# Optimization experiments

Measured on AMD Instinct MI355X. Metric: run time of the kernel, lower is better.

The kernel has to match this reference:

```python
import jax, jax.numpy as jnp
import numpy as np

B, T, D, H, C = 64, 256, 512, 1024, 1000

def setup_inputs() -> dict:
    key = jax.random.key(0)
    ks = jax.random.split(key, 6)
    s = 1.0 / np.sqrt(H)  # torch nn.RNN init scale
    return {
        "x": jax.random.normal(ks[0], (B, T, D), dtype=jnp.float32),
        "w_ih0": jax.random.normal(ks[1], (H, D), dtype=jnp.float32) * s,
        "w_hh0": jax.random.normal(ks[2], (H, H), dtype=jnp.float32) * s,
        "w_ih1": jax.random.normal(ks[3], (H, H), dtype=jnp.float32) * s,
        "w_hh1": jax.random.normal(ks[4], (H, H), dtype=jnp.float32) * s,
        "w_fc": jax.random.normal(ks[5], (C, H), dtype=jnp.float32) * s,
    }

def _rnn_layer(inp, w_ih, w_hh):
    # inp: [B, T, Din]; ReLU RNN, no bias (matches nn.RNN(nonlinearity='relu', bias=False))
    xs = jnp.einsum('btd,hd->tbh', inp, w_ih)  # precompute input projections for all steps
    h0 = jnp.zeros((inp.shape[0], w_hh.shape[0]), dtype=inp.dtype)
    def step(h, x_t):
        h = jax.nn.relu(x_t + h @ w_hh.T)
        return h, h
    _, ys = jax.lax.scan(step, h0, xs)  # ys: [T, B, H]
    return jnp.swapaxes(ys, 0, 1)  # [B, T, H]

def reference(x, w_ih0, w_hh0, w_ih1, w_hh1, w_fc):
    h1 = _rnn_layer(x, w_ih0, w_hh0)
    h2 = _rnn_layer(h1, w_ih1, w_hh1)
    # fc on last timestep, no bias
    return h2[:, -1, :] @ w_fc.T  # [B, C]
```

## Files before the change

kernel.cpp:

```cpp
#include <hip/hip_runtime.h>

#define T_STEPS 256
#define BATCH   64
#define HID     1024
#define DIN     512
#define NCLS    1000
#define NBLK    128
#define HSZ     (BATCH * HID)
#define POLL_MAX 100000L

typedef __attribute__((ext_vector_type(8))) short  short8;
typedef __attribute__((ext_vector_type(4))) float  f32x4;
typedef unsigned long long u64;

__device__ __forceinline__ unsigned short rne_bf16(float f) {
    unsigned int u = __builtin_bit_cast(unsigned int, f);
    u += 0x7FFFu + ((u >> 16) & 1u);
    return (unsigned short)(u >> 16);
}
__device__ __forceinline__ float bf16_to_f(unsigned short h) {
    unsigned int u = ((unsigned int)h) << 16;
    return __builtin_bit_cast(float, u);
}

#define MFMA(a, b, c) __builtin_amdgcn_mfma_f32_16x16x32_bf16((a), (b), (c), 0, 0, 0)

__device__ __forceinline__ short8 ld_st8(const unsigned short* p) {
    u64 a = __hip_atomic_load((const u64*)p,       __ATOMIC_RELAXED, __HIP_MEMORY_SCOPE_AGENT);
    u64 b = __hip_atomic_load((const u64*)(p + 4), __ATOMIC_RELAXED, __HIP_MEMORY_SCOPE_AGENT);
    union { u64 q[2]; short8 v; } u;
    u.q[0] = a; u.q[1] = b;
    return u.v;
}
__device__ __forceinline__ void st_u32(unsigned short* p, unsigned int v) {
    __hip_atomic_store((unsigned int*)p, v, __ATOMIC_RELAXED, __HIP_MEMORY_SCOPE_AGENT);
}

__device__ __forceinline__ void wave_poll(const int* fa, int ta,
                                          const int* fb, int tb, int lane) {
    const int* f = (lane < 32) ? fa : fb;
    const int  t = (lane < 32) ? ta : tb;
    const int  i = lane & 31;
    for (long it = 0; it < POLL_MAX; ++it) {
        int v = __hip_atomic_load(f + i, __ATOMIC_RELAXED, __HIP_MEMORY_SCOPE_AGENT);
        if (__all(v >= t)) break;
        __builtin_amdgcn_s_sleep(1);
    }
    asm volatile("" ::: "memory");
}

__global__ __launch_bounds__(512, 2)
void rnn_mfma(const float* __restrict__ xproj,
              const unsigned short* __restrict__ whh0h, const unsigned short* __restrict__ whh0l,
              const unsigned short* __restrict__ wih1h, const unsigned short* __restrict__ wih1l,
              const unsigned short* __restrict__ whh1h, const unsigned short* __restrict__ whh1l,
              unsigned short* h1hi, unsigned short* h1lo,
              unsigned short* h2hi, unsigned short* h2lo,
              float* h2f, int* bar) {
    __shared__ float red[8 * 1088];

    const int bid  = blockIdx.x;
    const int tid  = threadIdx.x;
    const int w    = tid >> 6;
    const int lane = tid & 63;
    const int l15  = lane & 15;
    const int kq   = (lane >> 4) * 8;
    const int rm   = tid >> 4;
    const int rn   = (tid * 2) & 31;

    const int isL2 = bid >= 64;
    const int rb   = isL2 ? bid - 64 : bid;
    const int ns   = rb >> 1;
    const int mh   = rb & 1;
    const int nb   = ns * 32;
    const int mb   = mh * 32;

    int* L1f = bar + mh * 32;
    int* L2f = bar + 64 + mh * 32;

    if (!isL2) {
        const int kb = w * 128;
        short8 WH[2][4], WL[2][4];
#pragma unroll
        for (int c = 0; c < 4; ++c)
#pragma unroll
            for (int nt = 0; nt < 2; ++nt) {
                const size_t o = (size_t)(nb + nt * 16 + l15) * HID + kb + c * 32 + kq;
                WH[nt][c] = *(const short8*)(whh0h + o);
                WL[nt][c] = *(const short8*)(whh0l + o);
            }
        for (int p = 0; p < T_STEPS; ++p) {
            const float2 xi = *(const float2*)(xproj + (size_t)p * BATCH * HID +
                                               (size_t)(mb + rm) * HID + nb + rn);
            wave_poll(L1f, p, L2f, p - 3, lane);
            const unsigned short* hch = h1hi + (size_t)(p & 3) * HSZ;
            const unsigned short* hcl = h1lo + (size_t)(p & 3) * HSZ;
            f32x4 acc[2][2] = {};
#pragma unroll
            for (int c = 0; c < 4; ++c) {
                short8 ah[2], al[2];
#pragma unroll
                for (int mt = 0; mt < 2; ++mt) {
                    const size_t o = (size_t)(mb + mt * 16 + l15) * HID + kb + c * 32 + kq;
                    ah[mt] = ld_st8(hch + o);
                    al[mt] = ld_st8(hcl + o);
                }
#pragma unroll
                for (int mt = 0; mt < 2; ++mt)
#pragma unroll
                    for (int nt = 0; nt < 2; ++nt) {
                        acc[mt][nt] = MFMA(ah[mt], WH[nt][c], acc[mt][nt]);
                        acc[mt][nt] = MFMA(al[mt], WH[nt][c], acc[mt][nt]);
                        acc[mt][nt] = MFMA(ah[mt], WL[nt][c], acc[mt][nt]);
                    }
            }
#pragma unroll
            for (int mt = 0; mt < 2; ++mt)
#pragma unroll
                for (int nt = 0; nt < 2; ++nt)
#pragma unroll
                    for (int i = 0; i < 4; ++i)
                        red[w * 1088 + (mt * 16 + (lane >> 4) * 4 + i) * 34 +
                            nt * 16 + l15] = acc[mt][nt][i];
            __syncthreads();
            {
                float s0 = xi.x, s1 = xi.y;
#pragma unroll
                for (int ww = 0; ww < 8; ++ww) {
                    const float* rp = red + ww * 1088 + rm * 34 + rn;
                    s0 += rp[0];
                    s1 += rp[1];
                }
                const float v0 = fmaxf(s0, 0.f), v1 = fmaxf(s1, 0.f);
                const unsigned short h0 = rne_bf16(v0), h1 = rne_bf16(v1);
                const unsigned int hp = (unsigned int)h0 | ((unsigned int)h1 << 16);
                const unsigned int lp = (unsigned int)rne_bf16(v0 - bf16_to_f(h0)) |
                                        ((unsigned int)rne_bf16(v1 - bf16_to_f(h1)) << 16);
                const size_t o  = (size_t)(mb + rm) * HID + nb + rn;
                const size_t ob = (size_t)((p + 1) & 3) * HSZ;
                st_u32(h1hi + ob + o, hp);
                st_u32(h1lo + ob + o, lp);
            }
            __syncthreads();
            if (tid == 0)
                __hip_atomic_store(&L1f[ns], p + 1, __ATOMIC_RELAXED,
                                   __HIP_MEMORY_SCOPE_AGENT);
        }
    } else {
        const unsigned short* ph = (w < 4) ? wih1h : whh1h;
        const unsigned short* pl = (w < 4) ? wih1l : whh1l;
        const int kb = (w & 3) * 256;
        short8 WH[2][8], WL[2][8];
#pragma unroll
        for (int c = 0; c < 8; ++c)
#pragma unroll
            for (int nt = 0; nt < 2; ++nt) {
                const size_t o = (size_t)(nb + nt * 16 + l15) * HID + kb + c * 32 + kq;
                WH[nt][c] = *(const short8*)(ph + o);
                WL[nt][c] = *(const short8*)(pl + o);
            }
        for (int p = 1; p <= T_STEPS; ++p) {
            if (w < 4) wave_poll(L1f, p, L1f, p, lane);
            else       wave_poll(L2f, p - 1, L2f, p - 1, lane);
            const unsigned short* ash = (w < 4) ? h1hi + (size_t)(p & 3) * HSZ
                                                : h2hi + (size_t)((p - 1) & 1) * HSZ;
            const unsigned short* asl = (w < 4) ? h1lo + (size_t)(p & 3) * HSZ
                                                : h2lo + (size_t)((p - 1) & 1) * HSZ;
            f32x4 acc[2][2] = {};
#pragma unroll
            for (int c = 0; c < 8; ++c) {
                short8 ah[2], al[2];
#pragma unroll
                for (int mt = 0; mt < 2; ++mt) {
                    const size_t o = (size_t)(mb + mt * 16 + l15) * HID + kb + c * 32 + kq;
                    ah[mt] = ld_st8(ash + o);
                    al[mt] = ld_st8(asl + o);
                }
#pragma unroll
                for (int mt = 0; mt < 2; ++mt)
#pragma unroll
                    for (int nt = 0; nt < 2; ++nt) {
                        acc[mt][nt] = MFMA(ah[mt], WH[nt][c], acc[mt][nt]);
                        acc[mt][nt] = MFMA(al[mt], WH[nt][c], acc[mt][nt]);
                        acc[mt][nt] = MFMA(ah[mt], WL[nt][c], acc[mt][nt]);
                    }
            }
#pragma unroll
            for (int mt = 0; mt < 2; ++mt)
#pragma unroll
                for (int nt = 0; nt < 2; ++nt)
#pragma unroll
                    for (int i = 0; i < 4; ++i)
                        red[w * 1088 + (mt * 16 + (lane >> 4) * 4 + i) * 34 +
                            nt * 16 + l15] = acc[mt][nt][i];
            __syncthreads();
            {
                float s0 = 0.f, s1 = 0.f;
#pragma unroll
                for (int ww = 0; ww < 8; ++ww) {
                    const float* rp = red + ww * 1088 + rm * 34 + rn;
                    s0 += rp[0];
                    s1 += rp[1];
                }
                const float v0 = fmaxf(s0, 0.f), v1 = fmaxf(s1, 0.f);
                const unsigned short h0 = rne_bf16(v0), h1 = rne_bf16(v1);
                const unsigned int hp = (unsigned int)h0 | ((unsigned int)h1 << 16);
                const unsigned int lp = (unsigned int)rne_bf16(v0 - bf16_to_f(h0)) |
                                        ((unsigned int)rne_bf16(v1 - bf16_to_f(h1)) << 16);
                const size_t o  = (size_t)(mb + rm) * HID + nb + rn;
                const size_t ob = (size_t)(p & 1) * HSZ;
                st_u32(h2hi + ob + o, hp);
                st_u32(h2lo + ob + o, lp);
                if (p == T_STEPS) {
                    float2 f2; f2.x = v0; f2.y = v1;
                    *(float2*)(h2f + o) = f2;
                }
            }
            __syncthreads();
            if (tid == 0)
                __hip_atomic_store(&L2f[ns], p, __ATOMIC_RELAXED,
                                   __HIP_MEMORY_SCOPE_AGENT);
        }
    }
}

__global__ __launch_bounds__(512)
void xproj_gemm(const float* __restrict__ x,
                const unsigned short* __restrict__ wh,
                const unsigned short* __restrict__ wl,
                float* __restrict__ xproj) {
    const int t    = blockIdx.x;
    const int nq   = blockIdx.y;
    const int w    = threadIdx.x >> 6;
    const int lane = threadIdx.x & 63;
    const int l15  = lane & 15;
    const int kq   = (lane >> 4) * 8;
    const int n0   = nq * 256 + w * 32;

    f32x4 acc[4][2] = {};
    for (int c = 0; c < 16; ++c) {
        const int k = c * 32 + kq;
        short8 wfh[2], wfl[2];
#pragma unroll
        for (int nt = 0; nt < 2; ++nt) {
            const size_t o = (size_t)(n0 + nt * 16 + l15) * DIN + k;
            wfh[nt] = *(const short8*)(wh + o);
            wfl[nt] = *(const short8*)(wl + o);
        }
#pragma unroll
        for (int mt = 0; mt < 4; ++mt) {
            const float* xr = x + ((size_t)(mt * 16 + l15) * T_STEPS + t) * DIN + k;
            float4 a0 = *(const float4*)xr;
            float4 a1 = *(const float4*)(xr + 4);
            float f[8] = {a0.x, a0.y, a0.z, a0.w, a1.x, a1.y, a1.z, a1.w};
            short8 ah, al;
#pragma unroll
            for (int i = 0; i < 8; ++i) {
                unsigned short h = rne_bf16(f[i]);
                ah[i] = (short)h;
                al[i] = (short)rne_bf16(f[i] - bf16_to_f(h));
            }
#pragma unroll
            for (int nt = 0; nt < 2; ++nt) {
                acc[mt][nt] = MFMA(ah, wfh[nt], acc[mt][nt]);
                acc[mt][nt] = MFMA(al, wfh[nt], acc[mt][nt]);
                acc[mt][nt] = MFMA(ah, wfl[nt], acc[mt][nt]);
            }
        }
    }
    float* op = xproj + (size_t)t * BATCH * HID;
#pragma unroll
    for (int mt = 0; mt < 4; ++mt)
#pragma unroll
        for (int nt = 0; nt < 2; ++nt)
#pragma unroll
            for (int i = 0; i < 4; ++i) {
                const int m = mt * 16 + (lane >> 4) * 4 + i;
                const int n = n0 + nt * 16 + l15;
                op[(size_t)m * HID + n] = acc[mt][nt][i];
            }
}

__global__ void split_w(const float* __restrict__ src,
                        unsigned short* __restrict__ hi,
                        unsigned short* __restrict__ lo, int n) {
    int i = blockIdx.x * 256 + threadIdx.x;
    if (i < n) {
        float v = src[i];
        unsigned short h = rne_bf16(v);
        hi[i] = h;
        lo[i] = rne_bf16(v - bf16_to_f(h));
    }
}

__global__ void zero_kernel(int* __restrict__ p, int n) {
    int i = blockIdx.x * 256 + threadIdx.x;
    if (i < n) p[i] = 0;
}

__global__ void fc_kernel(const float* __restrict__ h2,
                          const float* __restrict__ w_fc,
                          float* __restrict__ out) {
    __shared__ float hs[HID];
    const int b = blockIdx.x;
    for (int i = threadIdx.x; i < HID; i += 256) hs[i] = h2[(size_t)b * HID + i];
    __syncthreads();
    const int c = blockIdx.y * 256 + threadIdx.x;
    if (c < NCLS) {
        const float* w = w_fc + (size_t)c * HID;
        float s = 0.f;
        for (int k = 0; k < HID; k += 4) {
            float4 wv = *(const float4*)(w + k);
            s += wv.x * hs[k] + wv.y * hs[k + 1] + wv.z * hs[k + 2] + wv.w * hs[k + 3];
        }
        out[(size_t)b * NCLS + c] = s;
    }
}

extern "C" void kernel_launch(void* const* d_in, const int* in_sizes, int n_in,
                              void* d_out, int out_size, void* d_ws, size_t ws_size,
                              hipStream_t stream) {
    const float* x     = (const float*)d_in[0];
    const float* w_ih0 = (const float*)d_in[1];
    const float* w_hh0 = (const float*)d_in[2];
    const float* w_ih1 = (const float*)d_in[3];
    const float* w_hh1 = (const float*)d_in[4];
    const float* w_fc  = (const float*)d_in[5];
    float* out = (float*)d_out;

    char* ws = (char*)d_ws;
    size_t off = 0;
    auto alloc = [&](size_t bytes) { char* p = ws + off; off += bytes; return p; };
    float*          xproj = (float*)alloc((size_t)T_STEPS * BATCH * HID * 4);
    unsigned short* wih0h = (unsigned short*)alloc((size_t)DIN * HID * 2);
    unsigned short* wih0l = (unsigned short*)alloc((size_t)DIN * HID * 2);
    unsigned short* whh0h = (unsigned short*)alloc((size_t)HID * HID * 2);
    unsigned short* whh0l = (unsigned short*)alloc((size_t)HID * HID * 2);
    unsigned short* wih1h = (unsigned short*)alloc((size_t)HID * HID * 2);
    unsigned short* wih1l = (unsigned short*)alloc((size_t)HID * HID * 2);
    unsigned short* whh1h = (unsigned short*)alloc((size_t)HID * HID * 2);
    unsigned short* whh1l = (unsigned short*)alloc((size_t)HID * HID * 2);
    unsigned short* h1hi  = (unsigned short*)alloc(4 * HSZ * 2);
    unsigned short* h1lo  = (unsigned short*)alloc(4 * HSZ * 2);
    unsigned short* h2hi  = (unsigned short*)alloc(2 * HSZ * 2);
    unsigned short* h2lo  = (unsigned short*)alloc(2 * HSZ * 2);
    float*          h2f   = (float*)alloc(HSZ * 4);
    int*            bar   = (int*)alloc(4096);

    split_w<<<(DIN * HID + 255) / 256, 256, 0, stream>>>(w_ih0, wih0h, wih0l, DIN * HID);
    split_w<<<(HID * HID + 255) / 256, 256, 0, stream>>>(w_hh0, whh0h, whh0l, HID * HID);
    split_w<<<(HID * HID + 255) / 256, 256, 0, stream>>>(w_ih1, wih1h, wih1l, HID * HID);
    split_w<<<(HID * HID + 255) / 256, 256, 0, stream>>>(w_hh1, whh1h, whh1l, HID * HID);

    xproj_gemm<<<dim3(T_STEPS, 4), 512, 0, stream>>>(x, wih0h, wih0l, xproj);

    const int nzero = (4 * HSZ * 2 * 2 + 2 * HSZ * 2 * 2 + HSZ * 4 + 4096) / 4;
    zero_kernel<<<(nzero + 255) / 256, 256, 0, stream>>>((int*)h1hi, nzero);

    rnn_mfma<<<NBLK, 512, 0, stream>>>(xproj,
                                       whh0h, whh0l,
                                       wih1h, wih1l, whh1h, whh1l,
                                       h1hi, h1lo, h2hi, h2lo, h2f, bar);

    fc_kernel<<<dim3(64, 4), 256, 0, stream>>>(h2f, w_fc, out);
}
```

Before: 4.424 ms.

## Replace persistent flag-polling RNN kernel with per-step kernel launches

Replaces the single persistent kernel, which synchronized blocks through global flag polling and atomic loads and stores, with 257 launches of a step kernel. Each launch computes layer-1 step k and layer-2 step k-1, so the two layers stay wavefront-pipelined, with stream ordering acting as the barrier. This removes the spin-wait polling and the atomic memory traffic, and shrinks the h1 ring buffer from four slots to two. The cost is per-launch overhead, and each launch must reload the recurrent weights from global memory into registers.

```diff
diff --git a/kernel.cpp b/kernel.cpp
--- a/kernel.cpp
+++ b/kernel.cpp
@@ -7,11 +7,9 @@
 #define NCLS    1000
 #define NBLK    128
 #define HSZ     (BATCH * HID)
-#define POLL_MAX 100000L
 
 typedef __attribute__((ext_vector_type(8))) short  short8;
 typedef __attribute__((ext_vector_type(4))) float  f32x4;
-typedef unsigned long long u64;
 
 __device__ __forceinline__ unsigned short rne_bf16(float f) {
     unsigned int u = __builtin_bit_cast(unsigned int, f);
@@ -25,41 +23,22 @@
 
 #define MFMA(a, b, c) __builtin_amdgcn_mfma_f32_16x16x32_bf16((a), (b), (c), 0, 0, 0)
 
-__device__ __forceinline__ short8 ld_st8(const unsigned short* p) {
-    u64 a = __hip_atomic_load((const u64*)p,       __ATOMIC_RELAXED, __HIP_MEMORY_SCOPE_AGENT);
-    u64 b = __hip_atomic_load((const u64*)(p + 4), __ATOMIC_RELAXED, __HIP_MEMORY_SCOPE_AGENT);
-    union { u64 q[2]; short8 v; } u;
-    u.q[0] = a; u.q[1] = b;
-    return u.v;
-}
-__device__ __forceinline__ void st_u32(unsigned short* p, unsigned int v) {
-    __hip_atomic_store((unsigned int*)p, v, __ATOMIC_RELAXED, __HIP_MEMORY_SCOPE_AGENT);
-}
-
-__device__ __forceinline__ void wave_poll(const int* fa, int ta,
-                                          const int* fb, int tb, int lane) {
-    const int* f = (lane < 32) ? fa : fb;
-    const int  t = (lane < 32) ? ta : tb;
-    const int  i = lane & 31;
-    for (long it = 0; it < POLL_MAX; ++it) {
-        int v = __hip_atomic_load(f + i, __ATOMIC_RELAXED, __HIP_MEMORY_SCOPE_AGENT);
-        if (__all(v >= t)) break;
-        __builtin_amdgcn_s_sleep(1);
-    }
-    asm volatile("" ::: "memory");
-}
-
 __global__ __launch_bounds__(512, 2)
-void rnn_mfma(const float* __restrict__ xproj,
+void rnn_step(int k,
+              const float* __restrict__ xproj,
               const unsigned short* __restrict__ whh0h, const unsigned short* __restrict__ whh0l,
               const unsigned short* __restrict__ wih1h, const unsigned short* __restrict__ wih1l,
               const unsigned short* __restrict__ whh1h, const unsigned short* __restrict__ whh1l,
               unsigned short* h1hi, unsigned short* h1lo,
               unsigned short* h2hi, unsigned short* h2lo,
-              float* h2f, int* bar) {
+              float* h2f) {
     __shared__ float red[8 * 1088];
 
     const int bid  = blockIdx.x;
+    const int isL2 = bid >= 64;
+    if (!isL2 && k >= T_STEPS) return;
+    if (isL2 && k == 0)        return;
+
     const int tid  = threadIdx.x;
     const int w    = tid >> 6;
     const int lane = tid & 63;
@@ -68,15 +47,11 @@
     const int rm   = tid >> 4;
     const int rn   = (tid * 2) & 31;
 
-    const int isL2 = bid >= 64;
-    const int rb   = isL2 ? bid - 64 : bid;
-    const int ns   = rb >> 1;
-    const int mh   = rb & 1;
-    const int nb   = ns * 32;
-    const int mb   = mh * 32;
-
-    int* L1f = bar + mh * 32;
-    int* L2f = bar + 64 + mh * 32;
+    const int rb = isL2 ? bid - 64 : bid;
+    const int ns = rb >> 1;
+    const int mh = rb & 1;
+    const int nb = ns * 32;
+    const int mb = mh * 32;
 
     if (!isL2) {
         const int kb = w * 128;
@@ -89,62 +64,55 @@
                 WH[nt][c] = *(const short8*)(whh0h + o);
                 WL[nt][c] = *(const short8*)(whh0l + o);
             }
-        for (int p = 0; p < T_STEPS; ++p) {
-            const float2 xi = *(const float2*)(xproj + (size_t)p * BATCH * HID +
-                                               (size_t)(mb + rm) * HID + nb + rn);
-            wave_poll(L1f, p, L2f, p - 3, lane);
-            const unsigned short* hch = h1hi + (size_t)(p & 3) * HSZ;
-            const unsigned short* hcl = h1lo + (size_t)(p & 3) * HSZ;
-            f32x4 acc[2][2] = {};
-#pragma unroll
-            for (int c = 0; c < 4; ++c) {
-                short8 ah[2], al[2];
-#pragma unroll
-                for (int mt = 0; mt < 2; ++mt) {
-                    const size_t o = (size_t)(mb + mt * 16 + l15) * HID + kb + c * 32 + kq;
-                    ah[mt] = ld_st8(hch + o);
-                    al[mt] = ld_st8(hcl + o);
+        const float2 xi = *(const float2*)(xproj + (size_t)k * BATCH * HID +
+                                           (size_t)(mb + rm) * HID + nb + rn);
+        const unsigned short* hch = h1hi + (size_t)((k + 1) & 1) * HSZ;
+        const unsigned short* hcl = h1lo + (size_t)((k + 1) & 1) * HSZ;
+        f32x4 acc[2][2] = {};
+#pragma unroll
+        for (int c = 0; c < 4; ++c) {
+            short8 ah[2], al[2];
+#pragma unroll
+            for (int mt = 0; mt < 2; ++mt) {
+                const size_t o = (size_t)(mb + mt * 16 + l15) * HID + kb + c * 32 + kq;
+                ah[mt] = *(const short8*)(hch + o);
+                al[mt] = *(const short8*)(hcl + o);
+            }
+#pragma unroll
+            for (int mt = 0; mt < 2; ++mt)
+#pragma unroll
+                for (int nt = 0; nt < 2; ++nt) {
+                    acc[mt][nt] = MFMA(ah[mt], WH[nt][c], acc[mt][nt]);
+                    acc[mt][nt] = MFMA(al[mt], WH[nt][c], acc[mt][nt]);
+                    acc[mt][nt] = MFMA(ah[mt], WL[nt][c], acc[mt][nt]);
                 }
-#pragma unroll
-                for (int mt = 0; mt < 2; ++mt)
-#pragma unroll
-                    for (int nt = 0; nt < 2; ++nt) {
-                        acc[mt][nt] = MFMA(ah[mt], WH[nt][c], acc[mt][nt]);
-                        acc[mt][nt] = MFMA(al[mt], WH[nt][c], acc[mt][nt]);
-                        acc[mt][nt] = MFMA(ah[mt], WL[nt][c], acc[mt][nt]);
-                    }
-            }
-#pragma unroll
-            for (int mt = 0; mt < 2; ++mt)
-#pragma unroll
-                for (int nt = 0; nt < 2; ++nt)
-#pragma unroll
-                    for (int i = 0; i < 4; ++i)
-                        red[w * 1088 + (mt * 16 + (lane >> 4) * 4 + i) * 34 +
-                            nt * 16 + l15] = acc[mt][nt][i];
-            __syncthreads();
-            {
-                float s0 = xi.x, s1 = xi.y;
-#pragma unroll
-                for (int ww = 0; ww < 8; ++ww) {
-                    const float* rp = red + ww * 1088 + rm * 34 + rn;
-                    s0 += rp[0];
-                    s1 += rp[1];
-                }
-                const float v0 = fmaxf(s0, 0.f), v1 = fmaxf(s1, 0.f);
-                const unsigned short h0 = rne_bf16(v0), h1 = rne_bf16(v1);
-                const unsigned int hp = (unsigned int)h0 | ((unsigned int)h1 << 16);
-                const unsigned int lp = (unsigned int)rne_bf16(v0 - bf16_to_f(h0)) |
-                                        ((unsigned int)rne_bf16(v1 - bf16_to_f(h1)) << 16);
-                const size_t o  = (size_t)(mb + rm) * HID + nb + rn;
-                const size_t ob = (size_t)((p + 1) & 3) * HSZ;
-                st_u32(h1hi + ob + o, hp);
-                st_u32(h1lo + ob + o, lp);
-            }
-            __syncthreads();
-            if (tid == 0)
-                __hip_atomic_store(&L1f[ns], p + 1, __ATOMIC_RELAXED,
-                                   __HIP_MEMORY_SCOPE_AGENT);
+        }
+#pragma unroll
+        for (int mt = 0; mt < 2; ++mt)
+#pragma unroll
+            for (int nt = 0; nt < 2; ++nt)
+#pragma unroll
+                for (int i = 0; i < 4; ++i)
+                    red[w * 1088 + (mt * 16 + (lane >> 4) * 4 + i) * 34 +
+                        nt * 16 + l15] = acc[mt][nt][i];
+        __syncthreads();
+        {
+            float s0 = xi.x, s1 = xi.y;
+#pragma unroll
+            for (int ww = 0; ww < 8; ++ww) {
+                const float* rp = red + ww * 1088 + rm * 34 + rn;
+                s0 += rp[0];
+                s1 += rp[1];
+            }
+            const float v0 = fmaxf(s0, 0.f), v1 = fmaxf(s1, 0.f);
+            const unsigned short h0 = rne_bf16(v0), h1 = rne_bf16(v1);
+            const unsigned int hp = (unsigned int)h0 | ((unsigned int)h1 << 16);
+            const unsigned int lp = (unsigned int)rne_bf16(v0 - bf16_to_f(h0)) |
+                                    ((unsigned int)rne_bf16(v1 - bf16_to_f(h1)) << 16);
+            const size_t o  = (size_t)(mb + rm) * HID + nb + rn;
+            const size_t ob = (size_t)(k & 1) * HSZ;
+            *(unsigned int*)(h1hi + ob + o) = hp;
+            *(unsigned int*)(h1lo + ob + o) = lp;
         }
     } else {
         const unsigned short* ph = (w < 4) ? wih1h : whh1h;
@@ -159,67 +127,59 @@
                 WH[nt][c] = *(const short8*)(ph + o);
                 WL[nt][c] = *(const short8*)(pl + o);
             }
-        for (int p = 1; p <= T_STEPS; ++p) {
-            if (w < 4) wave_poll(L1f, p, L1f, p, lane);
-            else       wave_poll(L2f, p - 1, L2f, p - 1, lane);
-            const unsigned short* ash = (w < 4) ? h1hi + (size_t)(p & 3) * HSZ
-                                                : h2hi + (size_t)((p - 1) & 1) * HSZ;
-            const unsigned short* asl = (w < 4) ? h1lo + (size_t)(p & 3) * HSZ
-                                                : h2lo + (size_t)((p - 1) & 1) * HSZ;
-            f32x4 acc[2][2] = {};
-#pragma unroll
-            for (int c = 0; c < 8; ++c) {
-                short8 ah[2], al[2];
-#pragma unroll
-                for (int mt = 0; mt < 2; ++mt) {
-                    const size_t o = (size_t)(mb + mt * 16 + l15) * HID + kb + c * 32 + kq;
-                    ah[mt] = ld_st8(ash + o);
-                    al[mt] = ld_st8(asl + o);
+        const unsigned short* ash = (w < 4) ? h1hi + (size_t)((k + 1) & 1) * HSZ
+                                            : h2hi + (size_t)(k & 1) * HSZ;
+        const unsigned short* asl = (w < 4) ? h1lo + (size_t)((k + 1) & 1) * HSZ
+                                            : h2lo + (size_t)(k & 1) * HSZ;
+        f32x4 acc[2][2] = {};
+#pragma unroll
+        for (int c = 0; c < 8; ++c) {
+            short8 ah[2], al[2];
+#pragma unroll
+            for (int mt = 0; mt < 2; ++mt) {
+                const size_t o = (size_t)(mb + mt * 16 + l15) * HID + kb + c * 32 + kq;
+                ah[mt] = *(const short8*)(ash + o);
+                al[mt] = *(const short8*)(asl + o);
+            }
+#pragma unroll
+            for (int mt = 0; mt < 2; ++mt)
+#pragma unroll
+                for (int nt = 0; nt < 2; ++nt) {
+                    acc[mt][nt] = MFMA(ah[mt], WH[nt][c], acc[mt][nt]);
+                    acc[mt][nt] = MFMA(al[mt], WH[nt][c], acc[mt][nt]);
+                    acc[mt][nt] = MFMA(ah[mt], WL[nt][c], acc[mt][nt]);
                 }
-#pragma unroll
-                for (int mt = 0; mt < 2; ++mt)
-#pragma unroll
-                    for (int nt = 0; nt < 2; ++nt) {
-                        acc[mt][nt] = MFMA(ah[mt], WH[nt][c], acc[mt][nt]);
-                        acc[mt][nt] = MFMA(al[mt], WH[nt][c], acc[mt][nt]);
-                        acc[mt][nt] = MFMA(ah[mt], WL[nt][c], acc[mt][nt]);
-                    }
-            }
-#pragma unroll
-            for (int mt = 0; mt < 2; ++mt)
-#pragma unroll
-                for (int nt = 0; nt < 2; ++nt)
-#pragma unroll
-                    for (int i = 0; i < 4; ++i)
-                        red[w * 1088 + (mt * 16 + (lane >> 4) * 4 + i) * 34 +
-                            nt * 16 + l15] = acc[mt][nt][i];
-            __syncthreads();
-            {
-                float s0 = 0.f, s1 = 0.f;
-#pragma unroll
-                for (int ww = 0; ww < 8; ++ww) {
-                    const float* rp = red + ww * 1088 + rm * 34 + rn;
-                    s0 += rp[0];
-                    s1 += rp[1];
-                }
-                const float v0 = fmaxf(s0, 0.f), v1 = fmaxf(s1, 0.f);
-                const unsigned short h0 = rne_bf16(v0), h1 = rne_bf16(v1);
-                const unsigned int hp = (unsigned int)h0 | ((unsigned int)h1 << 16);
-                const unsigned int lp = (unsigned int)rne_bf16(v0 - bf16_to_f(h0)) |
-                                        ((unsigned int)rne_bf16(v1 - bf16_to_f(h1)) << 16);
-                const size_t o  = (size_t)(mb + rm) * HID + nb + rn;
-                const size_t ob = (size_t)(p & 1) * HSZ;
-                st_u32(h2hi + ob + o, hp);
-                st_u32(h2lo + ob + o, lp);
-                if (p == T_STEPS) {
-                    float2 f2; f2.x = v0; f2.y = v1;
-                    *(float2*)(h2f + o) = f2;
-                }
-            }
-            __syncthreads();
-            if (tid == 0)
-                __hip_atomic_store(&L2f[ns], p, __ATOMIC_RELAXED,
-                                   __HIP_MEMORY_SCOPE_AGENT);
+        }
+#pragma unroll
+        for (int mt = 0; mt < 2; ++mt)
+#pragma unroll
+            for (int nt = 0; nt < 2; ++nt)
+#pragma unroll
+                for (int i = 0; i < 4; ++i)
+                    red[w * 1088 + (mt * 16 + (lane >> 4) * 4 + i) * 34 +
+                        nt * 16 + l15] = acc[mt][nt][i];
+        __syncthreads();
+        {
+            float s0 = 0.f, s1 = 0.f;
+#pragma unroll
+            for (int ww = 0; ww < 8; ++ww) {
+                const float* rp = red + ww * 1088 + rm * 34 + rn;
+                s0 += rp[0];
+                s1 += rp[1];
+            }
+            const float v0 = fmaxf(s0, 0.f), v1 = fmaxf(s1, 0.f);
+            const unsigned short h0 = rne_bf16(v0), h1 = rne_bf16(v1);
+            const unsigned int hp = (unsigned int)h0 | ((unsigned int)h1 << 16);
+            const unsigned int lp = (unsigned int)rne_bf16(v0 - bf16_to_f(h0)) |
+                                    ((unsigned int)rne_bf16(v1 - bf16_to_f(h1)) << 16);
+            const size_t o  = (size_t)(mb + rm) * HID + nb + rn;
+            const size_t ob = (size_t)((k + 1) & 1) * HSZ;
+            *(unsigned int*)(h2hi + ob + o) = hp;
+            *(unsigned int*)(h2lo + ob + o) = lp;
+            if (k == T_STEPS) {
+                float2 f2; f2.x = v0; f2.y = v1;
+                *(float2*)(h2f + o) = f2;
+            }
         }
     }
 }
@@ -340,12 +300,11 @@
     unsigned short* wih1l = (unsigned short*)alloc((size_t)HID * HID * 2);
     unsigned short* whh1h = (unsigned short*)alloc((size_t)HID * HID * 2);
     unsigned short* whh1l = (unsigned short*)alloc((size_t)HID * HID * 2);
-    unsigned short* h1hi  = (unsigned short*)alloc(4 * HSZ * 2);
-    unsigned short* h1lo  = (unsigned short*)alloc(4 * HSZ * 2);
+    unsigned short* h1hi  = (unsigned short*)alloc(2 * HSZ * 2);
+    unsigned short* h1lo  = (unsigned short*)alloc(2 * HSZ * 2);
     unsigned short* h2hi  = (unsigned short*)alloc(2 * HSZ * 2);
     unsigned short* h2lo  = (unsigned short*)alloc(2 * HSZ * 2);
     float*          h2f   = (float*)alloc(HSZ * 4);
-    int*            bar   = (int*)alloc(4096);
 
     split_w<<<(DIN * HID + 255) / 256, 256, 0, stream>>>(w_ih0, wih0h, wih0l, DIN * HID);
     split_w<<<(HID * HID + 255) / 256, 256, 0, stream>>>(w_hh0, whh0h, whh0l, HID * HID);
@@ -354,13 +313,14 @@
 
     xproj_gemm<<<dim3(T_STEPS, 4), 512, 0, stream>>>(x, wih0h, wih0l, xproj);
 
-    const int nzero = (4 * HSZ * 2 * 2 + 2 * HSZ * 2 * 2 + HSZ * 4 + 4096) / 4;
+    const int nzero = (4 * (2 * HSZ * 2) + HSZ * 4) / 4;
     zero_kernel<<<(nzero + 255) / 256, 256, 0, stream>>>((int*)h1hi, nzero);
 
-    rnn_mfma<<<NBLK, 512, 0, stream>>>(xproj,
-                                       whh0h, whh0l,
-                                       wih1h, wih1l, whh1h, whh1l,
-                                       h1hi, h1lo, h2hi, h2lo, h2f, bar);
+    for (int k = 0; k <= T_STEPS; ++k)
+        rnn_step<<<NBLK, 512, 0, stream>>>(k, xproj,
+                                           whh0h, whh0l,
+                                           wih1h, wih1l, whh1h, whh1l,
+                                           h1hi, h1lo, h2hi, h2lo, h2f);
 
     fc_kernel<<<dim3(64, 4), 256, 0, stream>>>(h2f, w_fc, out);
 }
```

Result: slower. 4.575 ms (+3.4%).

## Replace shared barrier flags with per-block fan-out flag rows

Applied to the files above, without the earlier changes.

Each producer block now writes its progress counter into a dedicated row for every consumer block, using 64 threads. Each consumer polls only its own contiguous 64-int row with one load per lane. This is meant to reduce contention and cache-line sharing on the inter-block step barrier. The poll timeout is also lowered. Trade-offs: more flag stores per step, and every wave in a layer-2 block now waits on both dependencies.

```diff
diff --git a/kernel.cpp b/kernel.cpp
--- a/kernel.cpp
+++ b/kernel.cpp
@@ -7,7 +7,7 @@
 #define NCLS    1000
 #define NBLK    128
 #define HSZ     (BATCH * HID)
-#define POLL_MAX 100000L
+#define POLL_MAX 10000L
 
 typedef __attribute__((ext_vector_type(8))) short  short8;
 typedef __attribute__((ext_vector_type(4))) float  f32x4;
@@ -36,13 +36,10 @@
     __hip_atomic_store((unsigned int*)p, v, __ATOMIC_RELAXED, __HIP_MEMORY_SCOPE_AGENT);
 }
 
-__device__ __forceinline__ void wave_poll(const int* fa, int ta,
-                                          const int* fb, int tb, int lane) {
-    const int* f = (lane < 32) ? fa : fb;
-    const int  t = (lane < 32) ? ta : tb;
-    const int  i = lane & 31;
+__device__ __forceinline__ void poll_row(const int* row, int ta, int tb, int lane) {
+    const int t = (lane < 32) ? ta : tb;
     for (long it = 0; it < POLL_MAX; ++it) {
-        int v = __hip_atomic_load(f + i, __ATOMIC_RELAXED, __HIP_MEMORY_SCOPE_AGENT);
+        int v = __hip_atomic_load(row + lane, __ATOMIC_RELAXED, __HIP_MEMORY_SCOPE_AGENT);
         if (__all(v >= t)) break;
         __builtin_amdgcn_s_sleep(1);
     }
@@ -56,7 +53,7 @@
               const unsigned short* __restrict__ whh1h, const unsigned short* __restrict__ whh1l,
               unsigned short* h1hi, unsigned short* h1lo,
               unsigned short* h2hi, unsigned short* h2lo,
-              float* h2f, int* bar) {
+              float* h2f, int* flg) {
     __shared__ float red[8 * 1088];
 
     const int bid  = blockIdx.x;
@@ -75,8 +72,9 @@
     const int nb   = ns * 32;
     const int mb   = mh * 32;
 
-    int* L1f = bar + mh * 32;
-    int* L2f = bar + 64 + mh * 32;
+    const int* myrow = flg + bid * 64;
+    const int fan_c  = ((tid & 31) << 1) + mh + ((tid >= 32) ? 64 : 0);
+    int* fan_ptr = flg + fan_c * 64 + (isL2 ? 32 + ns : ns);
 
     if (!isL2) {
         const int kb = w * 128;
@@ -92,7 +90,7 @@
         for (int p = 0; p < T_STEPS; ++p) {
             const float2 xi = *(const float2*)(xproj + (size_t)p * BATCH * HID +
                                                (size_t)(mb + rm) * HID + nb + rn);
-            wave_poll(L1f, p, L2f, p - 3, lane);
+            poll_row(myrow, p, p - 3, lane);
             const unsigned short* hch = h1hi + (size_t)(p & 3) * HSZ;
             const unsigned short* hcl = h1lo + (size_t)(p & 3) * HSZ;
             f32x4 acc[2][2] = {};
@@ -142,8 +140,8 @@
                 st_u32(h1lo + ob + o, lp);
             }
             __syncthreads();
-            if (tid == 0)
-                __hip_atomic_store(&L1f[ns], p + 1, __ATOMIC_RELAXED,
+            if (tid < 64)
+                __hip_atomic_store(fan_ptr, p + 1, __ATOMIC_RELAXED,
                                    __HIP_MEMORY_SCOPE_AGENT);
         }
     } else {
@@ -160,8 +158,7 @@
                 WL[nt][c] = *(const short8*)(pl + o);
             }
         for (int p = 1; p <= T_STEPS; ++p) {
-            if (w < 4) wave_poll(L1f, p, L1f, p, lane);
-            else       wave_poll(L2f, p - 1, L2f, p - 1, lane);
+            poll_row(myrow, p, p - 1, lane);
             const unsigned short* ash = (w < 4) ? h1hi + (size_t)(p & 3) * HSZ
                                                 : h2hi + (size_t)((p - 1) & 1) * HSZ;
             const unsigned short* asl = (w < 4) ? h1lo + (size_t)(p & 3) * HSZ
@@ -217,8 +214,8 @@
                 }
             }
             __syncthreads();
-            if (tid == 0)
-                __hip_atomic_store(&L2f[ns], p, __ATOMIC_RELAXED,
+            if (tid < 64)
+                __hip_atomic_store(fan_ptr, p, __ATOMIC_RELAXED,
                                    __HIP_MEMORY_SCOPE_AGENT);
         }
     }
@@ -345,7 +342,7 @@
     unsigned short* h2hi  = (unsigned short*)alloc(2 * HSZ * 2);
     unsigned short* h2lo  = (unsigned short*)alloc(2 * HSZ * 2);
     float*          h2f   = (float*)alloc(HSZ * 4);
-    int*            bar   = (int*)alloc(4096);
+    int*            flg   = (int*)alloc(32768);
 
     split_w<<<(DIN * HID + 255) / 256, 256, 0, stream>>>(w_ih0, wih0h, wih0l, DIN * HID);
     split_w<<<(HID * HID + 255) / 256, 256, 0, stream>>>(w_hh0, whh0h, whh0l, HID * HID);
@@ -354,13 +351,13 @@
 
     xproj_gemm<<<dim3(T_STEPS, 4), 512, 0, stream>>>(x, wih0h, wih0l, xproj);
 
-    const int nzero = (4 * HSZ * 2 * 2 + 2 * HSZ * 2 * 2 + HSZ * 4 + 4096) / 4;
+    const int nzero = (4 * HSZ * 2 * 2 + 2 * HSZ * 2 * 2 + HSZ * 4 + 32768) / 4;
     zero_kernel<<<(nzero + 255) / 256, 256, 0, stream>>>((int*)h1hi, nzero);
 
     rnn_mfma<<<NBLK, 512, 0, stream>>>(xproj,
                                        whh0h, whh0l,
                                        wih1h, wih1l, whh1h, whh1l,
-                                       h1hi, h1lo, h2hi, h2lo, h2f, bar);
+                                       h1hi, h1lo, h2hi, h2lo, h2f, flg);
 
     fc_kernel<<<dim3(64, 4), 256, 0, stream>>>(h2f, w_fc, out);
 }
```

After: 4.359 ms. About the same (-1.5%).
